# Optimization experiments

Measured on AMD Instinct MI355X. Metric: run time of the kernel, lower is better.

## Reference

```python
import jax, jax.numpy as jnp
from jax import lax
import numpy as np

IN, H, T, NCLS = 256, 16, 10, 2
BN_EPS = 1e-5
NEG_SLOPE = 0.01


def _lstm_layer(x, w_ih, w_hh, b_ih, b_hh):
    # x: [B, T, D]; w_ih: [4H, D]; w_hh: [4H, H]; gates in torch order i,f,g,o
    B = x.shape[0]
    xg = jnp.einsum('btd,gd->btg', x, w_ih) + b_ih + b_hh  # [B, T, 4H]
    def step(carry, xt):
        h, c = carry
        g = xt + h @ w_hh.T
        i, f, gg, o = jnp.split(g, 4, axis=-1)
        c = jax.nn.sigmoid(f) * c + jax.nn.sigmoid(i) * jnp.tanh(gg)
        h = jax.nn.sigmoid(o) * jnp.tanh(c)
        return (h, c), h
    h0 = jnp.zeros((B, H), x.dtype)
    _, hs = lax.scan(step, (h0, h0), jnp.swapaxes(xg, 0, 1))  # [T, B, H]
    return jnp.swapaxes(hs, 0, 1)  # [B, T, H]


def setup_inputs() -> dict:
    key = jax.random.key(0)
    ks = jax.random.split(key, 12)
    s_ih0 = 1.0 / np.sqrt(IN); s_h = 1.0 / np.sqrt(H)
    inp = {
        'inputs': jax.random.normal(ks[0], (16384, T, IN), jnp.float32),
        'agegender': jax.random.normal(ks[1], (16384, 2), jnp.float32),
        # layer 0
        'w_ih0': jax.random.uniform(ks[2], (4 * H, IN), jnp.float32, -s_h, s_h),
        'w_hh0': jax.random.uniform(ks[3], (4 * H, H), jnp.float32, -s_h, s_h),
        'b_ih0': jax.random.uniform(ks[4], (4 * H,), jnp.float32, -s_h, s_h),
        'b_hh0': jax.random.uniform(ks[5], (4 * H,), jnp.float32, -s_h, s_h),
        # layer 1
        'w_ih1': jax.random.uniform(ks[6], (4 * H, H), jnp.float32, -s_h, s_h),
        'w_hh1': jax.random.uniform(ks[7], (4 * H, H), jnp.float32, -s_h, s_h),
        'b_ih1': jax.random.uniform(ks[8], (4 * H,), jnp.float32, -s_h, s_h),
        'b_hh1': jax.random.uniform(ks[9], (4 * H,), jnp.float32, -s_h, s_h),
        # BN(160) and FC(162 -> 2)
        'bn_gamma': jnp.ones((T * H,), jnp.float32),
        'bn_beta': jnp.zeros((T * H,), jnp.float32),
        'fc_w': jax.random.uniform(ks[10], (NCLS, T * H + 2), jnp.float32, -1.0 / np.sqrt(T * H + 2), 1.0 / np.sqrt(T * H + 2)),
        'fc_b': jax.random.uniform(ks[11], (NCLS,), jnp.float32, -1.0 / np.sqrt(T * H + 2), 1.0 / np.sqrt(T * H + 2)),
    }
    return inp


def reference(inputs, agegender, w_ih0, w_hh0, b_ih0, b_hh0,
              w_ih1, w_hh1, b_ih1, b_hh1, bn_gamma, bn_beta, fc_w, fc_b):
    h1 = _lstm_layer(inputs, w_ih0, w_hh0, b_ih0, b_hh0)   # [B, T, H]
    h2 = _lstm_layer(h1, w_ih1, w_hh1, b_ih1, b_hh1)       # [B, T, H]
    flat = h2.reshape(h2.shape[0], -1)                      # [B, 160]
    # BatchNorm1d in training mode: biased batch statistics
    mean = jnp.mean(flat, axis=0)
    var = jnp.var(flat, axis=0)
    xn = (flat - mean) * lax.rsqrt(var + BN_EPS) * bn_gamma + bn_beta
    act = jnp.where(xn >= 0, xn, NEG_SLOPE * xn)            # LeakyReLU
    cat = jnp.concatenate([act, agegender], axis=1)         # [B, 162]
    logits = cat @ fc_w.T + fc_b
    return jax.nn.softmax(logits, axis=1)
```

## Files before the change

kernel.cpp:

```cpp
#include <hip/hip_runtime.h>

#define NB 16384
#define TT 10
#define DIN 256
#define HH 16
#define NG 64
#define NF 160

typedef __attribute__((ext_vector_type(8))) _Float16 half8;
typedef __attribute__((ext_vector_type(4))) _Float16 half4;
typedef __attribute__((ext_vector_type(4))) float f32x4;
typedef unsigned int u32;

__device__ __forceinline__ void gld16(const float* g, float* l) {
    __builtin_amdgcn_global_load_lds(
        (const __attribute__((address_space(1))) u32*)g,
        (__attribute__((address_space(3))) u32*)l, 16, 0, 0);
}
__device__ __forceinline__ float sigf(float x) { return 1.0f / (1.0f + __expf(-x)); }
__device__ __forceinline__ float tanhf_(float x) {
    float e = __expf(2.0f * x);
    return 1.0f - 2.0f / (e + 1.0f);
}

__global__ __launch_bounds__(256) void k_prep(
        const float* __restrict__ w, const float* __restrict__ bi,
        const float* __restrict__ bh, const float* __restrict__ whh0,
        const float* __restrict__ wih1, const float* __restrict__ whh1,
        const float* __restrict__ bi1, const float* __restrict__ bh1,
        half8* __restrict__ Bf, float* __restrict__ bsum,
        half4* __restrict__ recw, float* __restrict__ b1s) {
    const int fi = blockIdx.x * 256 + threadIdx.x;
    {
        const int c = fi >> 9;
        const int s = (fi >> 6) & 7;
        const int ll = fi & 63;
        const int row = c * 16 + (ll & 15);
        const int k0 = s * 32 + ((ll >> 4) << 3);
        const float* wp = w + (size_t)row * DIN + k0;
        float4 a = *(const float4*)wp;
        float4 b = *(const float4*)(wp + 4);
        half8 h;
        h[0] = (_Float16)a.x; h[1] = (_Float16)a.y;
        h[2] = (_Float16)a.z; h[3] = (_Float16)a.w;
        h[4] = (_Float16)b.x; h[5] = (_Float16)b.y;
        h[6] = (_Float16)b.z; h[7] = (_Float16)b.w;
        Bf[fi] = h;
    }
    if (blockIdx.x < 3) {
        const float* M = blockIdx.x == 0 ? whh0 : (blockIdx.x == 1 ? wih1 : whh1);
        const int c = threadIdx.x >> 6;
        const int ll = threadIdx.x & 63;
        float4 v = *(const float4*)(M + (size_t)(c * 16 + (ll & 15)) * HH + ((ll >> 4) << 2));
        half4 h4;
        h4[0] = (_Float16)v.x; h4[1] = (_Float16)v.y;
        h4[2] = (_Float16)v.z; h4[3] = (_Float16)v.w;
        recw[blockIdx.x * 256 + c * 64 + ll] = h4;
    }
    if (blockIdx.x == 3 && threadIdx.x < NG) {
        bsum[threadIdx.x] = bi[threadIdx.x] + bh[threadIdx.x];
        b1s[threadIdx.x] = bi1[threadIdx.x] + bh1[threadIdx.x];
    }
}

__global__ __launch_bounds__(256, 1) void k_mega(
        const float* __restrict__ x, const half8* __restrict__ Bf,
        const float* __restrict__ bsum, const half4* __restrict__ recw,
        const float* __restrict__ b1s, _Float16* __restrict__ flatT) {
    __shared__ half8 Bl[2048];
    const int tid = threadIdx.x;
    const int l = tid & 63;
    const int wv = tid >> 6;

    #pragma unroll
    for (int q = 0; q < 8; ++q)
        gld16((const float*)(Bf + (wv * 8 + q) * 64 + l),
              (float*)(Bl + (wv * 8 + q) * 64));

    half4 w0f[4], w1f[4], w2f[4];
    f32x4 b0[4], b1[4];
    #pragma unroll
    for (int c = 0; c < 4; ++c) {
        w0f[c] = recw[0 * 256 + c * 64 + l];
        w1f[c] = recw[1 * 256 + c * 64 + l];
        w2f[c] = recw[2 * 256 + c * 64 + l];
        b0[c] = *(const f32x4*)(bsum + c * 16 + ((l >> 4) << 2));
        b1[c] = *(const f32x4*)(b1s + c * 16 + ((l >> 4) << 2));
    }
    __syncthreads();

    const int sb = blockIdx.x * 4 + wv;
    const float* xp = x + (size_t)(sb * 16 + (l & 15)) * TT * DIN + ((l >> 4) << 3);

    f32x4 A0[8], B0[8], A1[8], B1[8];
    #pragma unroll
    for (int s = 0; s < 8; ++s) {
        A0[s] = *(const f32x4*)(xp + s * 32);
        B0[s] = *(const f32x4*)(xp + s * 32 + 4);
    }

    half4 h0f, h1f;
    #pragma unroll
    for (int j = 0; j < 4; ++j) { h0f[j] = (_Float16)0.0f; h1f[j] = (_Float16)0.0f; }
    f32x4 cs0 = (f32x4)0.0f, cs1 = (f32x4)0.0f;

#define STEP(t, CA, CB, NA, NB2)                                               \
    {                                                                          \
        if ((t) < 9) {                                                         \
            _Pragma("unroll")                                                  \
            for (int s = 0; s < 8; ++s) {                                      \
                NA[s] = *(const f32x4*)(xp + ((t) + 1) * DIN + s * 32);        \
                NB2[s] = *(const f32x4*)(xp + ((t) + 1) * DIN + s * 32 + 4);   \
            }                                                                  \
        }                                                                      \
        f32x4 ac0[4] = {b0[0], b0[1], b0[2], b0[3]};                           \
        _Pragma("unroll")                                                      \
        for (int s = 0; s < 8; ++s) {                                          \
            float fv[8] = {CA[s].x, CA[s].y, CA[s].z, CA[s].w,                 \
                           CB[s].x, CB[s].y, CB[s].z, CB[s].w};                \
            half8 xh, xl;                                                      \
            _Pragma("unroll")                                                  \
            for (int j = 0; j < 8; ++j) {                                      \
                _Float16 hi = (_Float16)fv[j];                                 \
                xh[j] = hi;                                                    \
                xl[j] = (_Float16)(fv[j] - (float)hi);                         \
            }                                                                  \
            _Pragma("unroll")                                                  \
            for (int c = 0; c < 4; ++c) {                                      \
                half8 wf = Bl[(c * 8 + s) * 64 + l];                           \
                ac0[c] = __builtin_amdgcn_mfma_f32_16x16x32_f16(wf, xh, ac0[c], 0, 0, 0); \
                ac0[c] = __builtin_amdgcn_mfma_f32_16x16x32_f16(wf, xl, ac0[c], 0, 0, 0); \
            }                                                                  \
        }                                                                      \
        _Pragma("unroll")                                                      \
        for (int c = 0; c < 4; ++c)                                            \
            ac0[c] = __builtin_amdgcn_mfma_f32_16x16x16f16(w0f[c], h0f, ac0[c], 0, 0, 0); \
        f32x4 h0v;                                                             \
        _Pragma("unroll")                                                      \
        for (int r = 0; r < 4; ++r) {                                          \
            float iv = sigf(ac0[0][r]), fg = sigf(ac0[1][r]);                  \
            float gv = tanhf_(ac0[2][r]), ov = sigf(ac0[3][r]);                \
            cs0[r] = fg * cs0[r] + iv * gv;                                    \
            h0v[r] = ov * tanhf_(cs0[r]);                                      \
        }                                                                      \
        h0f[0] = (_Float16)h0v[0]; h0f[1] = (_Float16)h0v[1];                  \
        h0f[2] = (_Float16)h0v[2]; h0f[3] = (_Float16)h0v[3];                  \
        f32x4 ac1[4] = {b1[0], b1[1], b1[2], b1[3]};                           \
        _Pragma("unroll")                                                      \
        for (int c = 0; c < 4; ++c) {                                          \
            ac1[c] = __builtin_amdgcn_mfma_f32_16x16x16f16(w1f[c], h0f, ac1[c], 0, 0, 0); \
            ac1[c] = __builtin_amdgcn_mfma_f32_16x16x16f16(w2f[c], h1f, ac1[c], 0, 0, 0); \
        }                                                                      \
        f32x4 h1v;                                                             \
        _Pragma("unroll")                                                      \
        for (int r = 0; r < 4; ++r) {                                          \
            float iv = sigf(ac1[0][r]), fg = sigf(ac1[1][r]);                  \
            float gv = tanhf_(ac1[2][r]), ov = sigf(ac1[3][r]);                \
            cs1[r] = fg * cs1[r] + iv * gv;                                    \
            h1v[r] = ov * tanhf_(cs1[r]);                                      \
        }                                                                      \
        h1f[0] = (_Float16)h1v[0]; h1f[1] = (_Float16)h1v[1];                  \
        h1f[2] = (_Float16)h1v[2]; h1f[3] = (_Float16)h1v[3];                  \
        _Pragma("unroll")                                                      \
        for (int r = 0; r < 4; ++r)                                            \
            flatT[(size_t)((t) * 16 + ((l >> 4) << 2) + r) * NB + sb * 16 + (l & 15)] = (_Float16)h1v[r]; \
    }

    STEP(0, A0, B0, A1, B1)
    STEP(1, A1, B1, A0, B0)
    STEP(2, A0, B0, A1, B1)
    STEP(3, A1, B1, A0, B0)
    STEP(4, A0, B0, A1, B1)
    STEP(5, A1, B1, A0, B0)
    STEP(6, A0, B0, A1, B1)
    STEP(7, A1, B1, A0, B0)
    STEP(8, A0, B0, A1, B1)
    STEP(9, A1, B1, A0, B0)
#undef STEP
}

__global__ __launch_bounds__(256) void k_bn(
        const _Float16* __restrict__ flatT, const float* __restrict__ gamma,
        const float* __restrict__ beta, float* __restrict__ scale,
        float* __restrict__ shift) {
    const int f = blockIdx.x;
    const int tid = threadIdx.x;
    const _Float16* col = flatT + (size_t)f * NB;
    float s = 0.0f, q = 0.0f;
    #pragma unroll 8
    for (int i = tid; i < NB; i += 256) {
        float v = (float)col[i];
        s += v; q += v * v;
    }
    #pragma unroll
    for (int o = 32; o > 0; o >>= 1) {
        s += __shfl_down(s, o, 64);
        q += __shfl_down(q, o, 64);
    }
    __shared__ float rs[4], rq[4];
    const int wv = tid >> 6;
    if ((tid & 63) == 0) { rs[wv] = s; rq[wv] = q; }
    __syncthreads();
    if (tid == 0) {
        float S = rs[0] + rs[1] + rs[2] + rs[3];
        float Q = rq[0] + rq[1] + rq[2] + rq[3];
        float mean = S * (1.0f / NB);
        float var = Q * (1.0f / NB) - mean * mean;
        float sc = gamma[f] * rsqrtf(var + 1e-5f);
        scale[f] = sc;
        shift[f] = beta[f] - mean * sc;
    }
}

__global__ __launch_bounds__(256) void k_fc(
        const _Float16* __restrict__ flatT, const float* __restrict__ scale,
        const float* __restrict__ shift, const float* __restrict__ ag,
        const float* __restrict__ fcw, const float* __restrict__ fcb,
        float* __restrict__ out) {
    const int smp = blockIdx.x * 256 + threadIdx.x;
    float p0 = 0.0f, p1 = 0.0f;
    #pragma unroll 8
    for (int f = 0; f < NF; ++f) {
        float xn = (float)flatT[(size_t)f * NB + smp] * scale[f] + shift[f];
        float a = xn >= 0.0f ? xn : 0.01f * xn;
        p0 += a * fcw[f];
        p1 += a * fcw[162 + f];
    }
    float a0 = ag[(size_t)smp * 2 + 0], a1 = ag[(size_t)smp * 2 + 1];
    float l0 = p0 + a0 * fcw[160] + a1 * fcw[161] + fcb[0];
    float l1 = p1 + a0 * fcw[162 + 160] + a1 * fcw[162 + 161] + fcb[1];
    float m = fmaxf(l0, l1);
    float e0 = __expf(l0 - m), e1 = __expf(l1 - m);
    float inv = 1.0f / (e0 + e1);
    out[(size_t)smp * 2 + 0] = e0 * inv;
    out[(size_t)smp * 2 + 1] = e1 * inv;
}

extern "C" void kernel_launch(void* const* d_in, const int* in_sizes, int n_in,
                              void* d_out, int out_size, void* d_ws, size_t ws_size,
                              hipStream_t stream) {
    const float* x     = (const float*)d_in[0];
    const float* ag    = (const float*)d_in[1];
    const float* wih0  = (const float*)d_in[2];
    const float* whh0  = (const float*)d_in[3];
    const float* bih0  = (const float*)d_in[4];
    const float* bhh0  = (const float*)d_in[5];
    const float* wih1  = (const float*)d_in[6];
    const float* whh1  = (const float*)d_in[7];
    const float* bih1  = (const float*)d_in[8];
    const float* bhh1  = (const float*)d_in[9];
    const float* gamma = (const float*)d_in[10];
    const float* beta  = (const float*)d_in[11];
    const float* fcw   = (const float*)d_in[12];
    const float* fcb   = (const float*)d_in[13];
    float* out = (float*)d_out;

    float* ws = (float*)d_ws;
    _Float16* flatT = (_Float16*)ws;
    half8* Bf    = (half8*)(ws + 1310720);
    half4* recw  = (half4*)(ws + 1318912);
    float* bsum  = ws + 1320448;
    float* b1s   = ws + 1320512;
    float* scale = ws + 1320576;
    float* shift = ws + 1320736;

    k_prep<<<dim3(8),   dim3(256), 0, stream>>>(wih0, bih0, bhh0, whh0, wih1, whh1,
                                                bih1, bhh1, Bf, bsum, recw, b1s);
    k_mega<<<dim3(256), dim3(256), 0, stream>>>(x, Bf, bsum, recw, b1s, flatT);
    k_bn<<<dim3(NF),    dim3(256), 0, stream>>>(flatT, gamma, beta, scale, shift);
    k_fc<<<dim3(64),    dim3(256), 0, stream>>>(flatT, scale, shift, ag, fcw, fcb, out);
}
```

Before: 56.81 us.

## Split input projection K across two waves and fuse BN partial stats into LSTM kernel

The LSTM kernel now launches 1024 blocks of two waves, each block handling 16 sequences. The two waves split the 256-wide input projection in half and combine their partial gate sums through shared memory at every timestep. Wave 0 then runs the recurrent part and also reduces per-block BatchNorm sums and squared sums, which it writes out. The BN kernel reduces these 1024 partials instead of rescanning flatT. This adds memory parallelism and removes a pass over flatT, at the cost of two block barriers per step and wave 1 sitting idle during the recurrence.

```diff
diff --git a/kernel.cpp b/kernel.cpp
--- a/kernel.cpp
+++ b/kernel.cpp
@@ -63,19 +63,23 @@
     }
 }
 
-__global__ __launch_bounds__(256, 1) void k_mega(
+__global__ __launch_bounds__(128) void k_mega(
         const float* __restrict__ x, const half8* __restrict__ Bf,
         const float* __restrict__ bsum, const half4* __restrict__ recw,
-        const float* __restrict__ b1s, _Float16* __restrict__ flatT) {
+        const float* __restrict__ b1s, _Float16* __restrict__ flatT,
+        float* __restrict__ psumB, float* __restrict__ psqB) {
     __shared__ half8 Bl[2048];
+    __shared__ float exch[1024];
+    __shared__ float bnacc[NF];
+    __shared__ float bnsq[NF];
     const int tid = threadIdx.x;
     const int l = tid & 63;
-    const int wv = tid >> 6;
-
-    #pragma unroll
-    for (int q = 0; q < 8; ++q)
-        gld16((const float*)(Bf + (wv * 8 + q) * 64 + l),
-              (float*)(Bl + (wv * 8 + q) * 64));
+    const int kv = tid >> 6;
+
+    #pragma unroll
+    for (int q = 0; q < 16; ++q)
+        gld16((const float*)(Bf + q * 128 + kv * 64 + l),
+              (float*)(Bl + q * 128 + kv * 64));
 
     half4 w0f[4], w1f[4], w2f[4];
     f32x4 b0[4], b1[4];
@@ -89,12 +93,13 @@
     }
     __syncthreads();
 
-    const int sb = blockIdx.x * 4 + wv;
-    const float* xp = x + (size_t)(sb * 16 + (l & 15)) * TT * DIN + ((l >> 4) << 3);
-
-    f32x4 A0[8], B0[8], A1[8], B1[8];
-    #pragma unroll
-    for (int s = 0; s < 8; ++s) {
+    const int sb = blockIdx.x;
+    const float* xp = x + (size_t)(sb * 16 + (l & 15)) * TT * DIN
+                        + kv * 128 + ((l >> 4) << 3);
+
+    f32x4 A0[4], B0[4], A1[4], B1[4];
+    #pragma unroll
+    for (int s = 0; s < 4; ++s) {
         A0[s] = *(const f32x4*)(xp + s * 32);
         B0[s] = *(const f32x4*)(xp + s * 32 + 4);
     }
@@ -108,14 +113,16 @@
     {                                                                          \
         if ((t) < 9) {                                                         \
             _Pragma("unroll")                                                  \
-            for (int s = 0; s < 8; ++s) {                                      \
+            for (int s = 0; s < 4; ++s) {                                      \
                 NA[s] = *(const f32x4*)(xp + ((t) + 1) * DIN + s * 32);        \
                 NB2[s] = *(const f32x4*)(xp + ((t) + 1) * DIN + s * 32 + 4);   \
             }                                                                  \
         }                                                                      \
-        f32x4 ac0[4] = {b0[0], b0[1], b0[2], b0[3]};                           \
+        f32x4 ac0[4];                                                          \
         _Pragma("unroll")                                                      \
-        for (int s = 0; s < 8; ++s) {                                          \
+        for (int c = 0; c < 4; ++c) ac0[c] = kv ? (f32x4)0.0f : b0[c];         \
+        _Pragma("unroll")                                                      \
+        for (int s = 0; s < 4; ++s) {                                          \
             float fv[8] = {CA[s].x, CA[s].y, CA[s].z, CA[s].w,                 \
                            CB[s].x, CB[s].y, CB[s].z, CB[s].w};                \
             half8 xh, xl;                                                      \
@@ -127,43 +134,75 @@
             }                                                                  \
             _Pragma("unroll")                                                  \
             for (int c = 0; c < 4; ++c) {                                      \
-                half8 wf = Bl[(c * 8 + s) * 64 + l];                           \
+                half8 wf = Bl[(c * 8 + kv * 4 + s) * 64 + l];                  \
                 ac0[c] = __builtin_amdgcn_mfma_f32_16x16x32_f16(wf, xh, ac0[c], 0, 0, 0); \
                 ac0[c] = __builtin_amdgcn_mfma_f32_16x16x32_f16(wf, xl, ac0[c], 0, 0, 0); \
             }                                                                  \
         }                                                                      \
-        _Pragma("unroll")                                                      \
-        for (int c = 0; c < 4; ++c)                                            \
-            ac0[c] = __builtin_amdgcn_mfma_f32_16x16x16f16(w0f[c], h0f, ac0[c], 0, 0, 0); \
-        f32x4 h0v;                                                             \
-        _Pragma("unroll")                                                      \
-        for (int r = 0; r < 4; ++r) {                                          \
-            float iv = sigf(ac0[0][r]), fg = sigf(ac0[1][r]);                  \
-            float gv = tanhf_(ac0[2][r]), ov = sigf(ac0[3][r]);                \
-            cs0[r] = fg * cs0[r] + iv * gv;                                    \
-            h0v[r] = ov * tanhf_(cs0[r]);                                      \
+        if (kv == 1) {                                                         \
+            _Pragma("unroll")                                                  \
+            for (int c = 0; c < 4; ++c)                                        \
+                *(f32x4*)(exch + c * 256 + l * 4) = ac0[c];                    \
         }                                                                      \
-        h0f[0] = (_Float16)h0v[0]; h0f[1] = (_Float16)h0v[1];                  \
-        h0f[2] = (_Float16)h0v[2]; h0f[3] = (_Float16)h0v[3];                  \
-        f32x4 ac1[4] = {b1[0], b1[1], b1[2], b1[3]};                           \
-        _Pragma("unroll")                                                      \
-        for (int c = 0; c < 4; ++c) {                                          \
-            ac1[c] = __builtin_amdgcn_mfma_f32_16x16x16f16(w1f[c], h0f, ac1[c], 0, 0, 0); \
-            ac1[c] = __builtin_amdgcn_mfma_f32_16x16x16f16(w2f[c], h1f, ac1[c], 0, 0, 0); \
+        __syncthreads();                                                       \
+        if (kv == 0) {                                                         \
+            _Pragma("unroll")                                                  \
+            for (int c = 0; c < 4; ++c) {                                      \
+                f32x4 pr = *(const f32x4*)(exch + c * 256 + l * 4);            \
+                ac0[c].x += pr.x; ac0[c].y += pr.y;                            \
+                ac0[c].z += pr.z; ac0[c].w += pr.w;                            \
+                ac0[c] = __builtin_amdgcn_mfma_f32_16x16x16f16(w0f[c], h0f, ac0[c], 0, 0, 0); \
+            }                                                                  \
+            f32x4 h0v;                                                         \
+            _Pragma("unroll")                                                  \
+            for (int r = 0; r < 4; ++r) {                                      \
+                float iv = sigf(ac0[0][r]), fg = sigf(ac0[1][r]);              \
+                float gv = tanhf_(ac0[2][r]), ov = sigf(ac0[3][r]);            \
+                cs0[r] = fg * cs0[r] + iv * gv;                                \
+                h0v[r] = ov * tanhf_(cs0[r]);                                  \
+            }                                                                  \
+            h0f[0] = (_Float16)h0v[0]; h0f[1] = (_Float16)h0v[1];              \
+            h0f[2] = (_Float16)h0v[2]; h0f[3] = (_Float16)h0v[3];              \
+            f32x4 ac1[4] = {b1[0], b1[1], b1[2], b1[3]};                       \
+            _Pragma("unroll")                                                  \
+            for (int c = 0; c < 4; ++c) {                                      \
+                ac1[c] = __builtin_amdgcn_mfma_f32_16x16x16f16(w1f[c], h0f, ac1[c], 0, 0, 0); \
+                ac1[c] = __builtin_amdgcn_mfma_f32_16x16x16f16(w2f[c], h1f, ac1[c], 0, 0, 0); \
+            }                                                                  \
+            f32x4 h1v;                                                         \
+            _Pragma("unroll")                                                  \
+            for (int r = 0; r < 4; ++r) {                                      \
+                float iv = sigf(ac1[0][r]), fg = sigf(ac1[1][r]);              \
+                float gv = tanhf_(ac1[2][r]), ov = sigf(ac1[3][r]);            \
+                cs1[r] = fg * cs1[r] + iv * gv;                                \
+                h1v[r] = ov * tanhf_(cs1[r]);                                  \
+            }                                                                  \
+            h1f[0] = (_Float16)h1v[0]; h1f[1] = (_Float16)h1v[1];              \
+            h1f[2] = (_Float16)h1v[2]; h1f[3] = (_Float16)h1v[3];              \
+            _Pragma("unroll")                                                  \
+            for (int r = 0; r < 4; ++r)                                        \
+                flatT[(size_t)((t) * 16 + ((l >> 4) << 2) + r) * NB + sb * 16 + (l & 15)] = (_Float16)h1v[r]; \
+            f32x4 rs = h1v, rq;                                                \
+            _Pragma("unroll")                                                  \
+            for (int r = 0; r < 4; ++r) rq[r] = h1v[r] * h1v[r];               \
+            _Pragma("unroll")                                                  \
+            for (int m = 1; m < 16; m <<= 1) {                                 \
+                _Pragma("unroll")                                              \
+                for (int r = 0; r < 4; ++r) {                                  \
+                    rs[r] += __shfl_xor(rs[r], m, 16);                         \
+                    rq[r] += __shfl_xor(rq[r], m, 16);                         \
+                }                                                              \
+            }                                                                  \
+            if ((l & 15) == 0) {                                               \
+                const int rg = l >> 4;                                         \
+                _Pragma("unroll")                                              \
+                for (int r = 0; r < 4; ++r) {                                  \
+                    bnacc[(t) * 16 + rg * 4 + r] = rs[r];                      \
+                    bnsq[(t) * 16 + rg * 4 + r] = rq[r];                       \
+                }                                                              \
+            }                                                                  \
         }                                                                      \
-        f32x4 h1v;                                                             \
-        _Pragma("unroll")                                                      \
-        for (int r = 0; r < 4; ++r) {                                          \
-            float iv = sigf(ac1[0][r]), fg = sigf(ac1[1][r]);                  \
-            float gv = tanhf_(ac1[2][r]), ov = sigf(ac1[3][r]);                \
-            cs1[r] = fg * cs1[r] + iv * gv;                                    \
-            h1v[r] = ov * tanhf_(cs1[r]);                                      \
-        }                                                                      \
-        h1f[0] = (_Float16)h1v[0]; h1f[1] = (_Float16)h1v[1];                  \
-        h1f[2] = (_Float16)h1v[2]; h1f[3] = (_Float16)h1v[3];                  \
-        _Pragma("unroll")                                                      \
-        for (int r = 0; r < 4; ++r)                                            \
-            flatT[(size_t)((t) * 16 + ((l >> 4) << 2) + r) * NB + sb * 16 + (l & 15)] = (_Float16)h1v[r]; \
+        __syncthreads();                                                       \
     }
 
     STEP(0, A0, B0, A1, B1)
@@ -177,20 +216,25 @@
     STEP(8, A0, B0, A1, B1)
     STEP(9, A1, B1, A0, B0)
 #undef STEP
+
+    for (int f = tid; f < NF; f += 128) {
+        psumB[(size_t)sb * NF + f] = bnacc[f];
+        psqB[(size_t)sb * NF + f] = bnsq[f];
+    }
 }
 
 __global__ __launch_bounds__(256) void k_bn(
-        const _Float16* __restrict__ flatT, const float* __restrict__ gamma,
-        const float* __restrict__ beta, float* __restrict__ scale,
-        float* __restrict__ shift) {
+        const float* __restrict__ psumB, const float* __restrict__ psqB,
+        const float* __restrict__ gamma, const float* __restrict__ beta,
+        float* __restrict__ scale, float* __restrict__ shift) {
     const int f = blockIdx.x;
     const int tid = threadIdx.x;
-    const _Float16* col = flatT + (size_t)f * NB;
     float s = 0.0f, q = 0.0f;
-    #pragma unroll 8
-    for (int i = tid; i < NB; i += 256) {
-        float v = (float)col[i];
-        s += v; q += v * v;
+    #pragma unroll
+    for (int j = 0; j < 4; ++j) {
+        const int p = tid + j * 256;
+        s += psumB[(size_t)p * NF + f];
+        q += psqB[(size_t)p * NF + f];
     }
     #pragma unroll
     for (int o = 32; o > 0; o >>= 1) {
@@ -263,10 +307,13 @@
     float* b1s   = ws + 1320512;
     float* scale = ws + 1320576;
     float* shift = ws + 1320736;
-
-    k_prep<<<dim3(8),   dim3(256), 0, stream>>>(wih0, bih0, bhh0, whh0, wih1, whh1,
-                                                bih1, bhh1, Bf, bsum, recw, b1s);
-    k_mega<<<dim3(256), dim3(256), 0, stream>>>(x, Bf, bsum, recw, b1s, flatT);
-    k_bn<<<dim3(NF),    dim3(256), 0, stream>>>(flatT, gamma, beta, scale, shift);
-    k_fc<<<dim3(64),    dim3(256), 0, stream>>>(flatT, scale, shift, ag, fcw, fcb, out);
-}
+    float* psumB = ws + 1320896;
+    float* psqB  = ws + 1484736;
+
+    k_prep<<<dim3(8),    dim3(256), 0, stream>>>(wih0, bih0, bhh0, whh0, wih1, whh1,
+                                                 bih1, bhh1, Bf, bsum, recw, b1s);
+    k_mega<<<dim3(1024), dim3(128), 0, stream>>>(x, Bf, bsum, recw, b1s, flatT,
+                                                 psumB, psqB);
+    k_bn<<<dim3(NF),     dim3(256), 0, stream>>>(psumB, psqB, gamma, beta, scale, shift);
+    k_fc<<<dim3(64),     dim3(256), 0, stream>>>(flatT, scale, shift, ag, fcw, fcb, out);
+}
```

Result: slower. 66.05 us (+16.3%).

## Split LSTM timesteps across paired waves, staging second-half projections in LDS

Applied to the files above, without the earlier changes.

Each 16-sample group is now handled by a pair of waves. One wave computes the input projection plus recurrence for timesteps 0-4, while the other computes only the input projections for timesteps 5-9 and stores them in shared memory. After a block barrier, the first wave runs the recurrence for steps 5-9 from the staged projections. The grid doubles to 512 blocks and launch bounds allow 2 blocks per CU, raising parallelism on the heavy input-projection work, at the cost of about 40KB extra LDS, a barrier, and the partner wave sitting idle during the second recurrence phase.

```diff
diff --git a/kernel.cpp b/kernel.cpp
--- a/kernel.cpp
+++ b/kernel.cpp
@@ -63,19 +63,22 @@
     }
 }
 
-__global__ __launch_bounds__(256, 1) void k_mega(
+__global__ __launch_bounds__(256, 2) void k_mega(
         const float* __restrict__ x, const half8* __restrict__ Bf,
         const float* __restrict__ bsum, const half4* __restrict__ recw,
         const float* __restrict__ b1s, _Float16* __restrict__ flatT) {
     __shared__ half8 Bl[2048];
+    __shared__ float xgl[2][5120];
     const int tid = threadIdx.x;
     const int l = tid & 63;
-    const int wv = tid >> 6;
+    const int w = tid >> 6;
+    const int g = w >> 1;
+    const int role = w & 1;
 
     #pragma unroll
     for (int q = 0; q < 8; ++q)
-        gld16((const float*)(Bf + (wv * 8 + q) * 64 + l),
-              (float*)(Bl + (wv * 8 + q) * 64));
+        gld16((const float*)(Bf + (w * 8 + q) * 64 + l),
+              (float*)(Bl + (w * 8 + q) * 64));
 
     half4 w0f[4], w1f[4], w2f[4];
     f32x4 b0[4], b1[4];
@@ -89,8 +92,11 @@
     }
     __syncthreads();
 
-    const int sb = blockIdx.x * 4 + wv;
-    const float* xp = x + (size_t)(sb * 16 + (l & 15)) * TT * DIN + ((l >> 4) << 3);
+    const int sb = blockIdx.x * 2 + g;
+    const int tbase = role ? 5 : 0;
+    const float* xp = x + (size_t)(sb * 16 + (l & 15)) * TT * DIN
+                        + (size_t)tbase * DIN + ((l >> 4) << 3);
+    float* xgq = &xgl[g][0];
 
     f32x4 A0[8], B0[8], A1[8], B1[8];
     #pragma unroll
@@ -104,16 +110,14 @@
     for (int j = 0; j < 4; ++j) { h0f[j] = (_Float16)0.0f; h1f[j] = (_Float16)0.0f; }
     f32x4 cs0 = (f32x4)0.0f, cs1 = (f32x4)0.0f;
 
-#define STEP(t, CA, CB, NA, NB2)                                               \
-    {                                                                          \
-        if ((t) < 9) {                                                         \
+#define PROJ(i, CA, CB, NA, NB2, ac0)                                          \
+        if ((i) < 4) {                                                         \
             _Pragma("unroll")                                                  \
             for (int s = 0; s < 8; ++s) {                                      \
-                NA[s] = *(const f32x4*)(xp + ((t) + 1) * DIN + s * 32);        \
-                NB2[s] = *(const f32x4*)(xp + ((t) + 1) * DIN + s * 32 + 4);   \
+                NA[s] = *(const f32x4*)(xp + ((i) + 1) * DIN + s * 32);        \
+                NB2[s] = *(const f32x4*)(xp + ((i) + 1) * DIN + s * 32 + 4);   \
             }                                                                  \
         }                                                                      \
-        f32x4 ac0[4] = {b0[0], b0[1], b0[2], b0[3]};                           \
         _Pragma("unroll")                                                      \
         for (int s = 0; s < 8; ++s) {                                          \
             float fv[8] = {CA[s].x, CA[s].y, CA[s].z, CA[s].w,                 \
@@ -131,7 +135,9 @@
                 ac0[c] = __builtin_amdgcn_mfma_f32_16x16x32_f16(wf, xh, ac0[c], 0, 0, 0); \
                 ac0[c] = __builtin_amdgcn_mfma_f32_16x16x32_f16(wf, xl, ac0[c], 0, 0, 0); \
             }                                                                  \
-        }                                                                      \
+        }
+
+#define REC(gt, ac0)                                                           \
         _Pragma("unroll")                                                      \
         for (int c = 0; c < 4; ++c)                                            \
             ac0[c] = __builtin_amdgcn_mfma_f32_16x16x16f16(w0f[c], h0f, ac0[c], 0, 0, 0); \
@@ -163,20 +169,57 @@
         h1f[2] = (_Float16)h1v[2]; h1f[3] = (_Float16)h1v[3];                  \
         _Pragma("unroll")                                                      \
         for (int r = 0; r < 4; ++r)                                            \
-            flatT[(size_t)((t) * 16 + ((l >> 4) << 2) + r) * NB + sb * 16 + (l & 15)] = (_Float16)h1v[r]; \
-    }
-
-    STEP(0, A0, B0, A1, B1)
-    STEP(1, A1, B1, A0, B0)
-    STEP(2, A0, B0, A1, B1)
-    STEP(3, A1, B1, A0, B0)
-    STEP(4, A0, B0, A1, B1)
-    STEP(5, A1, B1, A0, B0)
-    STEP(6, A0, B0, A1, B1)
-    STEP(7, A1, B1, A0, B0)
-    STEP(8, A0, B0, A1, B1)
-    STEP(9, A1, B1, A0, B0)
-#undef STEP
+            flatT[(size_t)((gt) * 16 + ((l >> 4) << 2) + r) * NB + sb * 16 + (l & 15)] = (_Float16)h1v[r];
+
+    if (role == 0) {
+#define ASTEP(i, CA, CB, NA, NB2)                                              \
+        {                                                                      \
+            f32x4 ac0[4] = {b0[0], b0[1], b0[2], b0[3]};                       \
+            PROJ(i, CA, CB, NA, NB2, ac0)                                      \
+            REC(i, ac0)                                                        \
+        }
+        ASTEP(0, A0, B0, A1, B1)
+        ASTEP(1, A1, B1, A0, B0)
+        ASTEP(2, A0, B0, A1, B1)
+        ASTEP(3, A1, B1, A0, B0)
+        ASTEP(4, A0, B0, A1, B1)
+#undef ASTEP
+    } else {
+#define BSTEP(i, CA, CB, NA, NB2)                                              \
+        {                                                                      \
+            f32x4 ac0[4] = {b0[0], b0[1], b0[2], b0[3]};                       \
+            PROJ(i, CA, CB, NA, NB2, ac0)                                      \
+            _Pragma("unroll")                                                  \
+            for (int c = 0; c < 4; ++c)                                        \
+                *(f32x4*)(xgq + (i) * 1024 + c * 256 + l * 4) = ac0[c];        \
+        }
+        BSTEP(0, A0, B0, A1, B1)
+        BSTEP(1, A1, B1, A0, B0)
+        BSTEP(2, A0, B0, A1, B1)
+        BSTEP(3, A1, B1, A0, B0)
+        BSTEP(4, A0, B0, A1, B1)
+#undef BSTEP
+    }
+    __syncthreads();
+
+    if (role == 0) {
+#define TSTEP(tt)                                                              \
+        {                                                                      \
+            f32x4 ac0[4];                                                      \
+            _Pragma("unroll")                                                  \
+            for (int c = 0; c < 4; ++c)                                        \
+                ac0[c] = *(const f32x4*)(xgq + (tt) * 1024 + c * 256 + l * 4); \
+            REC((tt) + 5, ac0)                                                 \
+        }
+        TSTEP(0)
+        TSTEP(1)
+        TSTEP(2)
+        TSTEP(3)
+        TSTEP(4)
+#undef TSTEP
+    }
+#undef PROJ
+#undef REC
 }
 
 __global__ __launch_bounds__(256) void k_bn(
@@ -266,7 +309,7 @@
 
     k_prep<<<dim3(8),   dim3(256), 0, stream>>>(wih0, bih0, bhh0, whh0, wih1, whh1,
                                                 bih1, bhh1, Bf, bsum, recw, b1s);
-    k_mega<<<dim3(256), dim3(256), 0, stream>>>(x, Bf, bsum, recw, b1s, flatT);
+    k_mega<<<dim3(512), dim3(256), 0, stream>>>(x, Bf, bsum, recw, b1s, flatT);
     k_bn<<<dim3(NF),    dim3(256), 0, stream>>>(flatT, gamma, beta, scale, shift);
     k_fc<<<dim3(64),    dim3(256), 0, stream>>>(flatT, scale, shift, ag, fcw, fcb, out);
 }
```

Measured after the change: 87.93 us. 1.55x slower.
